# Performance work log

Measured on AMD Instinct MI355X. Metric: run time of the kernel, lower is better.

The kernel has to match this reference:

```python
import jax, jax.numpy as jnp
import numpy as np

N = 10000        # total nodes in batch
E = 320000       # total edges (before self-loops)
D_IN = 128       # node_dim
H_DIM = 64       # hidden_dim
HEADS = 4
B = 64           # number of graphs
NUM_EDGES = 1024 # actor output dim


def _lin(k, i, o):
    return jax.random.normal(k, (i, o), jnp.float32) / np.sqrt(i)


def setup_inputs() -> dict:
    key = jax.random.key(0)
    ks = jax.random.split(key, 32)
    x = jax.random.normal(ks[0], (N, D_IN), jnp.float32)
    edge_index = jax.random.randint(ks[1], (2, E), 0, N, dtype=jnp.int64)
    batch = jnp.sort(jax.random.randint(ks[2], (N,), 0, B, dtype=jnp.int64))
    inp = dict(x=x, edge_index=edge_index, batch=batch)
    # GAT layer 1: in=D_IN, heads=4, out=H_DIM, concat
    inp['W1'] = _lin(ks[3], D_IN, HEADS * H_DIM)
    inp['as1'] = jax.random.normal(ks[4], (HEADS, H_DIM), jnp.float32) * 0.1
    inp['ad1'] = jax.random.normal(ks[5], (HEADS, H_DIM), jnp.float32) * 0.1
    inp['b1'] = jnp.zeros((HEADS * H_DIM,), jnp.float32)
    # GAT layer 2: in=4*H_DIM, heads=4, out=H_DIM, concat
    inp['W2'] = _lin(ks[6], HEADS * H_DIM, HEADS * H_DIM)
    inp['as2'] = jax.random.normal(ks[7], (HEADS, H_DIM), jnp.float32) * 0.1
    inp['ad2'] = jax.random.normal(ks[8], (HEADS, H_DIM), jnp.float32) * 0.1
    inp['b2'] = jnp.zeros((HEADS * H_DIM,), jnp.float32)
    # GAT layer 3: in=4*H_DIM, heads=1, out=H_DIM, mean (concat=False)
    inp['W3'] = _lin(ks[9], HEADS * H_DIM, H_DIM)
    inp['as3'] = jax.random.normal(ks[10], (1, H_DIM), jnp.float32) * 0.1
    inp['ad3'] = jax.random.normal(ks[11], (1, H_DIM), jnp.float32) * 0.1
    inp['b3'] = jnp.zeros((H_DIM,), jnp.float32)
    # actor MLP
    inp['Wa1'] = _lin(ks[12], H_DIM, H_DIM); inp['ba1'] = jnp.zeros((H_DIM,), jnp.float32)
    inp['Wa2'] = _lin(ks[13], H_DIM, NUM_EDGES); inp['ba2'] = jnp.zeros((NUM_EDGES,), jnp.float32)
    # critic MLP
    inp['Wc1'] = _lin(ks[14], H_DIM, H_DIM); inp['bc1'] = jnp.zeros((H_DIM,), jnp.float32)
    inp['Wc2'] = _lin(ks[15], H_DIM, 1); inp['bc2'] = jnp.zeros((1,), jnp.float32)
    return inp


def gat_layer(x, src, dst, W, a_src, a_dst, bias, heads, out_dim, concat):
    # PyG GATConv: linear -> edge attention -> per-dst softmax -> scatter-add
    n = x.shape[0]
    h = (x @ W).reshape(n, heads, out_dim)            # [N,H,D]
    s = (h * a_src).sum(-1)                           # [N,H] attention src term
    d = (h * a_dst).sum(-1)                           # [N,H]
    e = jax.nn.leaky_relu(s[src] + d[dst], 0.2)       # [Eall,H]
    m = jax.ops.segment_max(e, dst, num_segments=n)   # stable softmax per dst node
    w = jnp.exp(e - m[dst])
    alpha = w / jax.ops.segment_sum(w, dst, num_segments=n)[dst]
    agg = jax.ops.segment_sum(h[src] * alpha[..., None], dst, num_segments=n)  # [N,H,D]
    o = agg.reshape(n, heads * out_dim) if concat else agg.mean(axis=1)
    return o + bias


def forward(x, edge_index, batch, W1, as1, ad1, b1, W2, as2, ad2, b2,
            W3, as3, ad3, b3, Wa1, ba1, Wa2, ba2, Wc1, bc1, Wc2, bc2):
    n = x.shape[0]
    loop = jnp.arange(n, dtype=edge_index.dtype)
    src = jnp.concatenate([edge_index[0], loop])      # add_self_loops=True (PyG default)
    dst = jnp.concatenate([edge_index[1], loop])
    h = jax.nn.relu(gat_layer(x, src, dst, W1, as1, ad1, b1, HEADS, H_DIM, True))
    h = jax.nn.relu(gat_layer(h, src, dst, W2, as2, ad2, b2, HEADS, H_DIM, True))
    h = jax.nn.relu(gat_layer(h, src, dst, W3, as3, ad3, b3, 1, H_DIM, False))
    # global_mean_pool
    counts = jax.ops.segment_sum(jnp.ones((n,), h.dtype), batch, num_segments=B)
    pooled = jax.ops.segment_sum(h, batch, num_segments=B) / jnp.maximum(counts, 1.0)[:, None]
    # heads (dropout is identity at inference)
    action = jnp.tanh(jax.nn.relu(pooled @ Wa1 + ba1) @ Wa2 + ba2)
    value = jax.nn.relu(pooled @ Wc1 + bc1) @ Wc2 + bc2
    return action, value


def reference(x, edge_index, batch, W1, as1, ad1, b1, W2, as2, ad2, b2,
              W3, as3, ad3, b3, Wa1, ba1, Wa2, ba2, Wc1, bc1, Wc2, bc2):
    return forward(x, edge_index, batch, W1, as1, ad1, b1, W2, as2, ad2, b2,
                   W3, as3, ad3, b3, Wa1, ba1, Wa2, ba2, Wc1, bc1, Wc2, bc2)
```

## Files before the change

### kernel.cpp

```cpp
#include <hip/hip_runtime.h>
#include <hip/hip_bf16.h>

#define NN 10000
#define EE 320000
#define EALL (EE + NN)
#define BG 64
#define AOUT 1024
#define CAP 128

#define WTOT 191361
#define SCB ((EALL + 255) / 256)

typedef __hip_bfloat16 bf16;
typedef __attribute__((ext_vector_type(8))) short bf16x8;
typedef __attribute__((ext_vector_type(4))) float f32x4;

__device__ __forceinline__ unsigned short f2bf(float f) {
    bf16 h = __float2bfloat16(f);
    return *reinterpret_cast<unsigned short*>(&h);
}
__device__ __forceinline__ float bf2f(unsigned short u) {
    bf16 h;
    *reinterpret_cast<unsigned short*>(&h) = u;
    return __bfloat162float(h);
}
__device__ __forceinline__ int iread(const void* p, int fi, long long idx) {
    return fi ? ((const int*)p)[idx] : (int)((const long long*)p)[idx];
}

struct WPtrs { const void* p[20]; };
#define CVT_TOT (WTOT + 32768 + 65536 + 16384 + NN)
__global__ __launch_bounds__(256) void k_cvt_all(WPtrs wp, const void* __restrict__ xsrc,
                          float* __restrict__ wf,
                          unsigned short* __restrict__ w1t, unsigned short* __restrict__ w2t,
                          unsigned short* __restrict__ w3t, int* __restrict__ cnt, int ffh) {
    __shared__ int sff;
    int ff = ffh;
    if (ffh < 0) {
        const int t = threadIdx.x;
        bool nanp = false;
        const uint4* xs4 = (const uint4*)xsrc;
        uint4 a = xs4[t * 8 + 0], b = xs4[t * 8 + 4];
        const unsigned int wds[8] = {a.x, a.y, a.z, a.w, b.x, b.y, b.z, b.w};
#pragma unroll
        for (int k = 0; k < 8; k++) {
            unsigned int w2 = wds[k];
            if ((w2 & 0x7F80u) == 0x7F80u || ((w2 >> 16) & 0x7F80u) == 0x7F80u) nanp = true;
        }
        unsigned long long bn = __ballot(nanp);
        if (t == 0) sff = 0;
        __syncthreads();
        if ((t & 63) == 0 && bn) atomicOr(&sff, 1);
        __syncthreads();
        ff = sff;
    }

    const int sz[20] = {32768,256,256,256,65536,256,256,256,16384,64,64,64,4096,64,65536,1024,4096,64,64,1};
    int i = blockIdx.x * 256 + threadIdx.x;
    if (i < WTOT) {
        int seg = 0, off = 0;
        while (i - off >= sz[seg]) { off += sz[seg]; seg++; }
        const void* src = wp.p[seg];
        int k = i - off;
        wf[i] = ff ? ((const float*)src)[k] : __bfloat162float(((const bf16*)src)[k]);
        return;
    }
    i -= WTOT;
    if (i < 32768) {
        int k = i >> 8, c = i & 255;
        float v = ff ? ((const float*)wp.p[0])[i] : __bfloat162float(((const bf16*)wp.p[0])[i]);
        w1t[c * 128 + k] = f2bf(v);
        return;
    }
    i -= 32768;
    if (i < 65536) {
        int k = i >> 8, c = i & 255;
        float v = ff ? ((const float*)wp.p[4])[i] : __bfloat162float(((const bf16*)wp.p[4])[i]);
        w2t[c * 256 + k] = f2bf(v);
        return;
    }
    i -= 65536;
    if (i < 16384) {
        int k = i >> 6, c = i & 63;
        float v = ff ? ((const float*)wp.p[8])[i] : __bfloat162float(((const bf16*)wp.p[8])[i]);
        w3t[c * 256 + k] = f2bf(v);
        return;
    }
    i -= 16384;
    if (i < NN) cnt[i] = 0;
}

__global__ __launch_bounds__(256) void k_fuse1(const void* __restrict__ eisrc,
                                               const void* __restrict__ xsrc,
                                               int ffh, int fih,
                                               int* __restrict__ cnt, int* __restrict__ ssrc,
                                               const unsigned short* __restrict__ WT16,
                                               const float* __restrict__ asf,
                                               const float* __restrict__ adf,
                                               unsigned short* __restrict__ C16,
                                               float* __restrict__ sb, float* __restrict__ db) {
    constexpr int LDW = 40;
    __shared__ alignas(16) char smem[10240];
    __shared__ int sff, sfi;
    const int t = threadIdx.x;
    int ff = ffh, fi = fih;
    if (ffh < 0 || fih < 0) {
        bool nanp = false, odd = false;
        const uint4* xs4 = (const uint4*)xsrc;
        uint4 a = xs4[t * 8 + 0], b = xs4[t * 8 + 4];
        const unsigned int wds[8] = {a.x, a.y, a.z, a.w, b.x, b.y, b.z, b.w};
#pragma unroll
        for (int k = 0; k < 8; k++) {
            unsigned int w2 = wds[k];
            if ((w2 & 0x7F80u) == 0x7F80u || ((w2 >> 16) & 0x7F80u) == 0x7F80u) nanp = true;
        }
        odd = ((const unsigned int*)eisrc)[2 * t + 1] != 0u;
        unsigned long long bn = __ballot(nanp);
        unsigned long long bo = __ballot(odd);
        if (t == 0) { sff = 0; sfi = 0; }
        __syncthreads();
        if ((t & 63) == 0) {
            if (bn) atomicOr(&sff, 1);
            if (bo) atomicOr(&sfi, 1);
        }
        __syncthreads();
        ff = (ffh >= 0) ? ffh : sff;
        fi = (fih >= 0) ? fih : sfi;
    }

    if (blockIdx.x < SCB) {
        int e = blockIdx.x * 256 + t;
        if (e < EALL) {
            int dst = (e < EE) ? iread(eisrc, fi, (long long)EE + e) : (e - EE);
            int src = (e < EE) ? iread(eisrc, fi, e) : dst;
            int pos = atomicAdd(&cnt[dst], 1);
            if (pos < CAP) ssrc[(size_t)dst * CAP + pos] = src;
        }
        return;
    }
    unsigned short* As = (unsigned short*)smem;
    unsigned short* Bs = As + 64 * LDW;
    constexpr int K = 128, M = 256, H = M / 64;
    const int u = blockIdx.x - SCB;
    const int bx = u % 157;
    const int hh = u / 157;
    const int row0 = bx * 64, col0 = hh * 64;
    const int wv = t >> 6, lane = t & 63;
    const int m = lane & 15, q = lane >> 4;
    const int srow = t >> 2, skoff = (t & 3) * 8;

    f32x4 acc[4] = {};
    for (int k0 = 0; k0 < K; k0 += 32) {
        {
            int grow = row0 + srow;
            uint4 av = make_uint4(0u, 0u, 0u, 0u);
            if (grow < NN) {
                if (ff) {
                    const float* xp = (const float*)xsrc + (size_t)grow * K + k0 + skoff;
                    float4 fa = *(const float4*)xp;
                    float4 fb = *(const float4*)(xp + 4);
                    union { unsigned short u16[8]; uint4 v; } pk;
                    pk.u16[0] = f2bf(fa.x); pk.u16[1] = f2bf(fa.y);
                    pk.u16[2] = f2bf(fa.z); pk.u16[3] = f2bf(fa.w);
                    pk.u16[4] = f2bf(fb.x); pk.u16[5] = f2bf(fb.y);
                    pk.u16[6] = f2bf(fb.z); pk.u16[7] = f2bf(fb.w);
                    av = pk.v;
                } else {
                    av = *(const uint4*)((const unsigned short*)xsrc + (size_t)grow * K + k0 + skoff);
                }
            }
            *(uint4*)&As[srow * LDW + skoff] = av;
            uint4 bv = *(const uint4*)&WT16[(size_t)(col0 + srow) * K + k0 + skoff];
            *(uint4*)&Bs[srow * LDW + skoff] = bv;
        }
        __syncthreads();
        bf16x8 af = *(const bf16x8*)&As[(16 * wv + m) * LDW + q * 8];
#pragma unroll
        for (int ct = 0; ct < 4; ct++) {
            bf16x8 bfv = *(const bf16x8*)&Bs[(16 * ct + m) * LDW + q * 8];
            acc[ct] = __builtin_amdgcn_mfma_f32_16x16x32_bf16(af, bfv, acc[ct], 0, 0, 0);
        }
        __syncthreads();
    }
    float asv[4], adv[4];
#pragma unroll
    for (int ct = 0; ct < 4; ct++) {
        asv[ct] = asf[hh * 64 + 16 * ct + m];
        adv[ct] = adf[hh * 64 + 16 * ct + m];
    }
#pragma unroll
    for (int reg = 0; reg < 4; reg++) {
        int row = row0 + 16 * wv + q * 4 + reg;
        float ps = 0.f, pd = 0.f;
        if (row < NN) {
#pragma unroll
            for (int ct = 0; ct < 4; ct++) {
                float v = acc[ct][reg];
                C16[(size_t)row * M + col0 + 16 * ct + m] = f2bf(v);
                ps += v * asv[ct];
                pd += v * adv[ct];
            }
        }
#pragma unroll
        for (int off = 1; off < 16; off <<= 1) {
            ps += __shfl_xor(ps, off);
            pd += __shfl_xor(pd, off);
        }
        if (m == 0 && row < NN) { sb[row * H + hh] = ps; db[row * H + hh] = pd; }
    }
}

template<int K, int M>
__global__ __launch_bounds__(256) void k_gemm(const unsigned short* __restrict__ A16,
                                              const unsigned short* __restrict__ WT16,
                                              const float* __restrict__ asf,
                                              const float* __restrict__ adf,
                                              unsigned short* __restrict__ C16,
                                              float* __restrict__ sb, float* __restrict__ db) {
    constexpr int BK = 32;
    constexpr int H = M / 64;
    constexpr int LDW = 40;
    __shared__ unsigned short As[64 * LDW];
    __shared__ unsigned short Bs[64 * LDW];
    const int row0 = blockIdx.x * 64;
    const int col0 = blockIdx.y * 64;
    const int hh = blockIdx.y;
    const int t = threadIdx.x;
    const int wv = t >> 6;
    const int lane = t & 63;
    const int m = lane & 15;
    const int q = lane >> 4;
    const int srow = t >> 2;
    const int skoff = (t & 3) * 8;

    f32x4 acc[4] = {};

    for (int k0 = 0; k0 < K; k0 += BK) {
        {
            int grow = row0 + srow;
            uint4 av = make_uint4(0u, 0u, 0u, 0u);
            if (grow < NN) av = *(const uint4*)&A16[(size_t)grow * K + k0 + skoff];
            *(uint4*)&As[srow * LDW + skoff] = av;
            uint4 bv = *(const uint4*)&WT16[(size_t)(col0 + srow) * K + k0 + skoff];
            *(uint4*)&Bs[srow * LDW + skoff] = bv;
        }
        __syncthreads();
        bf16x8 af = *(const bf16x8*)&As[(16 * wv + m) * LDW + q * 8];
#pragma unroll
        for (int ct = 0; ct < 4; ct++) {
            bf16x8 bfv = *(const bf16x8*)&Bs[(16 * ct + m) * LDW + q * 8];
            acc[ct] = __builtin_amdgcn_mfma_f32_16x16x32_bf16(af, bfv, acc[ct], 0, 0, 0);
        }
        __syncthreads();
    }

    float asv[4], adv[4];
#pragma unroll
    for (int ct = 0; ct < 4; ct++) {
        asv[ct] = asf[hh * 64 + 16 * ct + m];
        adv[ct] = adf[hh * 64 + 16 * ct + m];
    }
#pragma unroll
    for (int reg = 0; reg < 4; reg++) {
        int row = row0 + 16 * wv + q * 4 + reg;
        float ps = 0.f, pd = 0.f;
        if (row < NN) {
#pragma unroll
            for (int ct = 0; ct < 4; ct++) {
                float v = acc[ct][reg];
                C16[(size_t)row * M + col0 + 16 * ct + m] = f2bf(v);
                ps += v * asv[ct];
                pd += v * adv[ct];
            }
        }
#pragma unroll
        for (int off = 1; off < 16; off <<= 1) {
            ps += __shfl_xor(ps, off);
            pd += __shfl_xor(pd, off);
        }
        if (m == 0 && row < NN) { sb[row * H + hh] = ps; db[row * H + hh] = pd; }
    }
}

template<int H>
__global__ void k_agg(const unsigned short* __restrict__ hbuf16, const float* __restrict__ sb,
                      const float* __restrict__ db, const int* __restrict__ cnt,
                      const int* __restrict__ ssrc, const float* __restrict__ bias,
                      unsigned short* __restrict__ out16) {
    constexpr int M = H * 64;
    constexpr int NW = M / 64;
    constexpr int CG = M / 8;
    constexpr int LCG = (H == 4) ? 5 : 3;
    const int n = blockIdx.x;
    const int tid = threadIdx.x;
    const int start = n * CAP;
    const int end = start + min(cnt[n], CAP);
    const int wv = tid >> 6;
    const int lane = tid & 63;
    const int cg = tid & (CG - 1);
    const int eg = tid >> LCG;
    const int chh = (H == 4) ? (cg >> 3) : 0;
    __shared__ float accbuf[8 * M];
    __shared__ float sww[NW][H];
    const float dn = db[n * H + chh];

    float wsum = 0.f;
    float acc[8] = {};
#pragma unroll 4
    for (int p = start + eg; p < end; p += 8) {
        int s = ssrc[p];
        float e = sb[s * H + chh] + dn;
        e = e > 0.f ? e : 0.2f * e;
        float w2 = __expf(e);
        wsum += w2;
        const bf16x8 v = *(const bf16x8*)&hbuf16[(size_t)s * M + cg * 8];
#pragma unroll
        for (int i = 0; i < 8; i++)
            acc[i] += w2 * bf2f((unsigned short)v[i]);
    }

    {
        float* ab = &accbuf[eg * M + cg * 8];
#pragma unroll
        for (int i = 0; i < 8; i++) ab[i] = acc[i];
    }
    if constexpr (NW > 1) {
        wsum += __shfl_xor(wsum, 32);
        if (lane < 32 && (cg & 7) == 0) sww[wv][chh] = wsum;
    } else {
        wsum += __shfl_xor(wsum, 8);
        wsum += __shfl_xor(wsum, 16);
        wsum += __shfl_xor(wsum, 32);
    }
    __syncthreads();

    float wsh;
    if constexpr (NW > 1) {
        const int h2 = tid >> 6;
        wsh = sww[0][h2] + sww[1][h2] + sww[2][h2] + sww[3][h2];
    } else {
        wsh = wsum;
    }

    float o = 0.f;
#pragma unroll
    for (int e8 = 0; e8 < 8; e8++) o += accbuf[e8 * M + tid];
    o = o / wsh + bias[tid];
    out16[(size_t)n * M + tid] = f2bf(fmaxf(o, 0.f));
}

__global__ __launch_bounds__(256) void k_final(const unsigned short* __restrict__ feat16,
                                               const void* __restrict__ bsrc, int fih,
                                               const void* __restrict__ eisrc,
                                               const float* __restrict__ Wa1, const float* __restrict__ ba1,
                                               const float* __restrict__ Wc1, const float* __restrict__ bc1,
                                               const float* __restrict__ Wa2, const float* __restrict__ ba2,
                                               const float* __restrict__ Wc2, const float* __restrict__ bc2,
                                               float* __restrict__ out) {
    __shared__ float red[256];
    __shared__ float p[64];
    __shared__ float a[64], cc[64];
    __shared__ int sfi;
    const int g = blockIdx.x, t = threadIdx.x;
    int fi = fih;
    if (fih < 0) {
        bool odd = ((const unsigned int*)eisrc)[2 * t + 1] != 0u;
        unsigned long long bo = __ballot(odd);
        if (t == 0) sfi = 0;
        __syncthreads();
        if ((t & 63) == 0 && bo) atomicOr(&sfi, 1);
        __syncthreads();
        fi = sfi;
    }
    int s, e;
    {
        int lo = 0, hi = NN;
        while (lo < hi) { int mid = (lo + hi) >> 1; if (iread(bsrc, fi, mid) < g) lo = mid + 1; else hi = mid; }
        s = lo;
        lo = 0; hi = NN;
        while (lo < hi) { int mid = (lo + hi) >> 1; if (iread(bsrc, fi, mid) < g + 1) lo = mid + 1; else hi = mid; }
        e = lo;
    }
    const int d = t & 63, c = t >> 6;
    float acc = 0.f;
    for (int n = s + c; n < e; n += 4) acc += bf2f(feat16[(size_t)n * 64 + d]);
    red[t] = acc; __syncthreads();
    if (c == 0) p[d] = (red[d] + red[64 + d] + red[128 + d] + red[192 + d])
                       / fmaxf((float)(e - s), 1.f);
    __syncthreads();
    if (t < 128) {
        int j = t & 63;
        const float* W  = (t < 64) ? Wa1 : Wc1;
        const float* bb = (t < 64) ? ba1 : bc1;
        float h = 0.f;
#pragma unroll 8
        for (int k = 0; k < 64; k++) h += p[k] * W[k * 64 + j];
        h = fmaxf(h + bb[j], 0.f);
        if (t < 64) a[j] = h; else cc[j] = h;
    }
    __syncthreads();
    float o[4] = {0.f, 0.f, 0.f, 0.f};
    for (int k = 0; k < 64; k++) {
        float ak = a[k];
#pragma unroll
        for (int q = 0; q < 4; q++) o[q] += ak * Wa2[k * AOUT + t + 256 * q];
    }
#pragma unroll
    for (int q = 0; q < 4; q++)
        out[g * AOUT + t + 256 * q] = tanhf(o[q] + ba2[t + 256 * q]);
    if (t == 0) {
        float v = 0.f;
        for (int k = 0; k < 64; k++) v += cc[k] * Wc2[k];
        out[BG * AOUT + g] = v + bc2[0];
    }
}

extern "C" void kernel_launch(void* const* d_in, const int* in_sizes, int n_in,
                              void* d_out, int out_size, void* d_ws, size_t ws_size,
                              hipStream_t stream) {
    float* out = (float*)d_out;

    char* w = (char*)d_ws;
    auto alloc = [&](size_t bytes) { void* p = (void*)w; w += (bytes + 255) & ~size_t(255); return p; };
    float* wf      = (float*)alloc((size_t)WTOT * 4);
    unsigned short* w1t    = (unsigned short*)alloc((size_t)32768 * 2);
    unsigned short* w2t    = (unsigned short*)alloc((size_t)65536 * 2);
    unsigned short* w3t    = (unsigned short*)alloc((size_t)16384 * 2);
    unsigned short* actA16 = (unsigned short*)alloc((size_t)NN * 256 * 2);
    unsigned short* actB16 = (unsigned short*)alloc((size_t)NN * 256 * 2);
    float* sb      = (float*)alloc((size_t)NN * 4 * 4);
    float* db      = (float*)alloc((size_t)NN * 4 * 4);
    int*   cnt     = (int*)alloc((size_t)NN * 4);
    int*   ssrc    = (int*)alloc((size_t)NN * CAP * 4);

    int ffh = -1, fih = -1;
    if (in_sizes && n_in >= 2) {
        long long xs = in_sizes[0];
        if (xs == (long long)NN * 128 * 4) ffh = 1;
        else if (xs == (long long)NN * 128 * 2) ffh = 0;
        long long es = in_sizes[1];
        if (es == (long long)2 * EE * 8) fih = 0;
        else if (es == (long long)2 * EE * 4) fih = 1;
    }

    WPtrs wp;
    for (int s = 0; s < 20; s++) wp.p[s] = d_in[3 + s];
    k_cvt_all<<<(CVT_TOT + 255) / 256, 256, 0, stream>>>(
        wp, d_in[0], wf, w1t, w2t, w3t, cnt, ffh);

    const int wsz[20] = {32768,256,256,256,65536,256,256,256,16384,64,64,64,4096,64,65536,1024,4096,64,64,1};
    int woff[20]; int acc = 0;
    for (int s = 0; s < 20; s++) { woff[s] = acc; acc += wsz[s]; }
    const float *as1f = wf + woff[1], *ad1f = wf + woff[2], *b1f = wf + woff[3];
    const float *as2f = wf + woff[5], *ad2f = wf + woff[6], *b2f = wf + woff[7];
    const float *as3f = wf + woff[9], *ad3f = wf + woff[10], *b3f = wf + woff[11];
    const float *Wa1f = wf + woff[12], *ba1f = wf + woff[13], *Wa2f = wf + woff[14], *ba2f = wf + woff[15];
    const float *Wc1f = wf + woff[16], *bc1f = wf + woff[17], *Wc2f = wf + woff[18], *bc2f = wf + woff[19];

    k_fuse1<<<SCB + 628, 256, 0, stream>>>(d_in[1], d_in[0], ffh, fih, cnt, ssrc,
                                           w1t, as1f, ad1f, actA16, sb, db);

    k_agg<4><<<NN, 256, 0, stream>>>(actA16, sb, db, cnt, ssrc, b1f, actB16);

    k_gemm<256, 256><<<dim3(157, 4), 256, 0, stream>>>(actB16, w2t, as2f, ad2f, actA16, sb, db);
    k_agg<4><<<NN, 256, 0, stream>>>(actA16, sb, db, cnt, ssrc, b2f, actB16);

    k_gemm<256, 64><<<dim3(157, 1), 256, 0, stream>>>(actB16, w3t, as3f, ad3f, actA16, sb, db);
    k_agg<1><<<NN, 64, 0, stream>>>(actA16, sb, db, cnt, ssrc, b3f, actB16);

    k_final<<<BG, 256, 0, stream>>>(actB16, d_in[2], fih, d_in[1],
                                    Wa1f, ba1f, Wc1f, bc1f, Wa2f, ba2f, Wc2f, bc2f, out);
}
```

Measured before the change: 224.5 us.

## Widen aggregation blocks, pack layer-3 nodes per block, skip large weight conversion

The 4-head aggregation now runs 512 threads per node with 16 edge groups, which is meant to expose more memory parallelism per node. The single-head aggregation packs four nodes per 256-thread block, one wave each, and drops the block-level sync, which is meant to raise occupancy and shrink the grid. The conversion kernel now converts only the small attention and bias vectors. The head MLP weights are read directly in their native dtype inside the final kernel, which now also detects the dtype itself, so the bulk fp32 copy of about 190K weights goes away. In exchange, half the threads in each 4-head block sit idle during the final reduction, and the final kernel carries extra dtype-branching code.

Result: slower. 238.2 us (+6.1%).

```diff
diff --git a/kernel.cpp b/kernel.cpp
--- a/kernel.cpp
+++ b/kernel.cpp
@@ -8,7 +8,6 @@
 #define AOUT 1024
 #define CAP 128
 
-#define WTOT 191361
 #define SCB ((EALL + 255) / 256)
 
 typedef __hip_bfloat16 bf16;
@@ -27,11 +26,14 @@
 __device__ __forceinline__ int iread(const void* p, int fi, long long idx) {
     return fi ? ((const int*)p)[idx] : (int)((const long long*)p)[idx];
 }
+__device__ __forceinline__ float fread1(const void* p, int ff, int idx) {
+    return ff ? ((const float*)p)[idx] : bf2f(((const unsigned short*)p)[idx]);
+}
 
 struct WPtrs { const void* p[20]; };
-#define CVT_TOT (WTOT + 32768 + 65536 + 16384 + NN)
+#define CVT_TOT (1728 + 32768 + 65536 + 16384 + NN)
 __global__ __launch_bounds__(256) void k_cvt_all(WPtrs wp, const void* __restrict__ xsrc,
-                          float* __restrict__ wf,
+                          float* __restrict__ wfv,
                           unsigned short* __restrict__ w1t, unsigned short* __restrict__ w2t,
                           unsigned short* __restrict__ w3t, int* __restrict__ cnt, int ffh) {
     __shared__ int sff;
@@ -55,34 +57,35 @@
         ff = sff;
     }
 
-    const int sz[20] = {32768,256,256,256,65536,256,256,256,16384,64,64,64,4096,64,65536,1024,4096,64,64,1};
     int i = blockIdx.x * 256 + threadIdx.x;
-    if (i < WTOT) {
+    if (i < 1728) {
+        const int vsz[9]  = {256,256,256,256,256,256,64,64,64};
+        const int vwp[9]  = {1,2,3,5,6,7,9,10,11};
+        const int voff[9] = {0,256,512,768,1024,1280,1536,1600,1664};
         int seg = 0, off = 0;
-        while (i - off >= sz[seg]) { off += sz[seg]; seg++; }
-        const void* src = wp.p[seg];
+        while (i - off >= vsz[seg]) { off += vsz[seg]; seg++; }
         int k = i - off;
-        wf[i] = ff ? ((const float*)src)[k] : __bfloat162float(((const bf16*)src)[k]);
+        wfv[voff[seg] + k] = fread1(wp.p[vwp[seg]], ff, k);
         return;
     }
-    i -= WTOT;
+    i -= 1728;
     if (i < 32768) {
         int k = i >> 8, c = i & 255;
-        float v = ff ? ((const float*)wp.p[0])[i] : __bfloat162float(((const bf16*)wp.p[0])[i]);
+        float v = fread1(wp.p[0], ff, i);
         w1t[c * 128 + k] = f2bf(v);
         return;
     }
     i -= 32768;
     if (i < 65536) {
         int k = i >> 8, c = i & 255;
-        float v = ff ? ((const float*)wp.p[4])[i] : __bfloat162float(((const bf16*)wp.p[4])[i]);
+        float v = fread1(wp.p[4], ff, i);
         w2t[c * 256 + k] = f2bf(v);
         return;
     }
     i -= 65536;
     if (i < 16384) {
         int k = i >> 6, c = i & 63;
-        float v = ff ? ((const float*)wp.p[8])[i] : __bfloat162float(((const bf16*)wp.p[8])[i]);
+        float v = fread1(wp.p[8], ff, i);
         w3t[c * 256 + k] = f2bf(v);
         return;
     }
@@ -282,95 +285,144 @@
     }
 }
 
-template<int H>
-__global__ void k_agg(const unsigned short* __restrict__ hbuf16, const float* __restrict__ sb,
-                      const float* __restrict__ db, const int* __restrict__ cnt,
-                      const int* __restrict__ ssrc, const float* __restrict__ bias,
-                      unsigned short* __restrict__ out16) {
-    constexpr int M = H * 64;
-    constexpr int NW = M / 64;
-    constexpr int CG = M / 8;
-    constexpr int LCG = (H == 4) ? 5 : 3;
+__global__ __launch_bounds__(512) void k_agg4(const unsigned short* __restrict__ hbuf16,
+                                              const float* __restrict__ sb,
+                                              const float* __restrict__ db,
+                                              const int* __restrict__ cnt,
+                                              const int* __restrict__ ssrc,
+                                              const float* __restrict__ bias,
+                                              unsigned short* __restrict__ out16) {
     const int n = blockIdx.x;
     const int tid = threadIdx.x;
     const int start = n * CAP;
     const int end = start + min(cnt[n], CAP);
-    const int wv = tid >> 6;
-    const int lane = tid & 63;
-    const int cg = tid & (CG - 1);
-    const int eg = tid >> LCG;
-    const int chh = (H == 4) ? (cg >> 3) : 0;
-    __shared__ float accbuf[8 * M];
-    __shared__ float sww[NW][H];
-    const float dn = db[n * H + chh];
-
+    const int wv = tid >> 6, lane = tid & 63;
+    const int cg = tid & 31;
+    const int eg = tid >> 5;
+    const int chh = cg >> 3;
+    __shared__ float accbuf[16 * 256];
+    __shared__ float sww[8][4];
+    const float dn = db[n * 4 + chh];
+
+    float wsum = 0.f;
+    float acc[8] = {};
+#pragma unroll 2
+    for (int p = start + eg; p < end; p += 16) {
+        int s = ssrc[p];
+        float e = sb[s * 4 + chh] + dn;
+        e = e > 0.f ? e : 0.2f * e;
+        float w2 = __expf(e);
+        wsum += w2;
+        const bf16x8 v = *(const bf16x8*)&hbuf16[(size_t)s * 256 + cg * 8];
+#pragma unroll
+        for (int i = 0; i < 8; i++)
+            acc[i] += w2 * bf2f((unsigned short)v[i]);
+    }
+    {
+        float* ab = &accbuf[eg * 256 + cg * 8];
+#pragma unroll
+        for (int i = 0; i < 8; i++) ab[i] = acc[i];
+    }
+    wsum += __shfl_xor(wsum, 32);
+    if (lane < 32 && (cg & 7) == 0) sww[wv][chh] = wsum;
+    __syncthreads();
+
+    if (tid < 256) {
+        const int h2 = tid >> 6;
+        float wsh = 0.f;
+#pragma unroll
+        for (int wq = 0; wq < 8; wq++) wsh += sww[wq][h2];
+        float o = 0.f;
+#pragma unroll
+        for (int e8 = 0; e8 < 16; e8++) o += accbuf[e8 * 256 + tid];
+        o = o / wsh + bias[tid];
+        out16[(size_t)n * 256 + tid] = f2bf(fmaxf(o, 0.f));
+    }
+}
+
+__global__ __launch_bounds__(256) void k_agg1w(const unsigned short* __restrict__ hbuf16,
+                                               const float* __restrict__ sb,
+                                               const float* __restrict__ db,
+                                               const int* __restrict__ cnt,
+                                               const int* __restrict__ ssrc,
+                                               const float* __restrict__ bias,
+                                               unsigned short* __restrict__ out16) {
+    __shared__ float accb[4 * 512];
+    const int tid = threadIdx.x;
+    const int wv = tid >> 6, lane = tid & 63;
+    const int eg = lane >> 3, cg = lane & 7;
+    const int n = blockIdx.x * 4 + wv;
+    if (n >= NN) return;
+    const int start = n * CAP;
+    const int end = start + min(cnt[n], CAP);
+    const float dn = db[n];
     float wsum = 0.f;
     float acc[8] = {};
 #pragma unroll 4
     for (int p = start + eg; p < end; p += 8) {
         int s = ssrc[p];
-        float e = sb[s * H + chh] + dn;
+        float e = sb[s] + dn;
         e = e > 0.f ? e : 0.2f * e;
         float w2 = __expf(e);
         wsum += w2;
-        const bf16x8 v = *(const bf16x8*)&hbuf16[(size_t)s * M + cg * 8];
+        const bf16x8 v = *(const bf16x8*)&hbuf16[(size_t)s * 64 + cg * 8];
 #pragma unroll
         for (int i = 0; i < 8; i++)
             acc[i] += w2 * bf2f((unsigned short)v[i]);
     }
-
     {
-        float* ab = &accbuf[eg * M + cg * 8];
+        float* ab = &accb[wv * 512 + eg * 64 + cg * 8];
 #pragma unroll
         for (int i = 0; i < 8; i++) ab[i] = acc[i];
     }
-    if constexpr (NW > 1) {
-        wsum += __shfl_xor(wsum, 32);
-        if (lane < 32 && (cg & 7) == 0) sww[wv][chh] = wsum;
-    } else {
-        wsum += __shfl_xor(wsum, 8);
-        wsum += __shfl_xor(wsum, 16);
-        wsum += __shfl_xor(wsum, 32);
-    }
-    __syncthreads();
-
-    float wsh;
-    if constexpr (NW > 1) {
-        const int h2 = tid >> 6;
-        wsh = sww[0][h2] + sww[1][h2] + sww[2][h2] + sww[3][h2];
-    } else {
-        wsh = wsum;
-    }
-
+    wsum += __shfl_xor(wsum, 8);
+    wsum += __shfl_xor(wsum, 16);
+    wsum += __shfl_xor(wsum, 32);
     float o = 0.f;
 #pragma unroll
-    for (int e8 = 0; e8 < 8; e8++) o += accbuf[e8 * M + tid];
-    o = o / wsh + bias[tid];
-    out16[(size_t)n * M + tid] = f2bf(fmaxf(o, 0.f));
+    for (int e8 = 0; e8 < 8; e8++) o += accb[wv * 512 + e8 * 64 + lane];
+    o = o / wsum + bias[lane];
+    out16[(size_t)n * 64 + lane] = f2bf(fmaxf(o, 0.f));
 }
 
 __global__ __launch_bounds__(256) void k_final(const unsigned short* __restrict__ feat16,
-                                               const void* __restrict__ bsrc, int fih,
+                                               const void* __restrict__ bsrc,
                                                const void* __restrict__ eisrc,
-                                               const float* __restrict__ Wa1, const float* __restrict__ ba1,
-                                               const float* __restrict__ Wc1, const float* __restrict__ bc1,
-                                               const float* __restrict__ Wa2, const float* __restrict__ ba2,
-                                               const float* __restrict__ Wc2, const float* __restrict__ bc2,
+                                               const void* __restrict__ xsrc,
+                                               int ffh, int fih,
+                                               const void* __restrict__ Wa1, const void* __restrict__ ba1,
+                                               const void* __restrict__ Wa2, const void* __restrict__ ba2,
+                                               const void* __restrict__ Wc1, const void* __restrict__ bc1,
+                                               const void* __restrict__ Wc2, const void* __restrict__ bc2,
                                                float* __restrict__ out) {
     __shared__ float red[256];
     __shared__ float p[64];
     __shared__ float a[64], cc[64];
-    __shared__ int sfi;
+    __shared__ int sff, sfi;
     const int g = blockIdx.x, t = threadIdx.x;
-    int fi = fih;
-    if (fih < 0) {
-        bool odd = ((const unsigned int*)eisrc)[2 * t + 1] != 0u;
+    int ff = ffh, fi = fih;
+    if (ffh < 0 || fih < 0) {
+        bool nanp = false, odd = false;
+        const uint4* xs4 = (const uint4*)xsrc;
+        uint4 av = xs4[t * 8 + 0], bv = xs4[t * 8 + 4];
+        const unsigned int wds[8] = {av.x, av.y, av.z, av.w, bv.x, bv.y, bv.z, bv.w};
+#pragma unroll
+        for (int k = 0; k < 8; k++) {
+            unsigned int w2 = wds[k];
+            if ((w2 & 0x7F80u) == 0x7F80u || ((w2 >> 16) & 0x7F80u) == 0x7F80u) nanp = true;
+        }
+        odd = ((const unsigned int*)eisrc)[2 * t + 1] != 0u;
+        unsigned long long bn = __ballot(nanp);
         unsigned long long bo = __ballot(odd);
-        if (t == 0) sfi = 0;
-        __syncthreads();
-        if ((t & 63) == 0 && bo) atomicOr(&sfi, 1);
-        __syncthreads();
-        fi = sfi;
+        if (t == 0) { sff = 0; sfi = 0; }
+        __syncthreads();
+        if ((t & 63) == 0) {
+            if (bn) atomicOr(&sff, 1);
+            if (bo) atomicOr(&sfi, 1);
+        }
+        __syncthreads();
+        ff = (ffh >= 0) ? ffh : sff;
+        fi = (fih >= 0) ? fih : sfi;
     }
     int s, e;
     {
@@ -390,28 +442,45 @@
     __syncthreads();
     if (t < 128) {
         int j = t & 63;
-        const float* W  = (t < 64) ? Wa1 : Wc1;
-        const float* bb = (t < 64) ? ba1 : bc1;
+        const void* W  = (t < 64) ? Wa1 : Wc1;
+        const void* bb = (t < 64) ? ba1 : bc1;
         float h = 0.f;
+        if (ff) {
+            const float* Wf = (const float*)W;
 #pragma unroll 8
-        for (int k = 0; k < 64; k++) h += p[k] * W[k * 64 + j];
-        h = fmaxf(h + bb[j], 0.f);
+            for (int k = 0; k < 64; k++) h += p[k] * Wf[k * 64 + j];
+        } else {
+            const unsigned short* Wh = (const unsigned short*)W;
+#pragma unroll 8
+            for (int k = 0; k < 64; k++) h += p[k] * bf2f(Wh[k * 64 + j]);
+        }
+        h = fmaxf(h + fread1(bb, ff, j), 0.f);
         if (t < 64) a[j] = h; else cc[j] = h;
     }
     __syncthreads();
     float o[4] = {0.f, 0.f, 0.f, 0.f};
-    for (int k = 0; k < 64; k++) {
-        float ak = a[k];
-#pragma unroll
-        for (int q = 0; q < 4; q++) o[q] += ak * Wa2[k * AOUT + t + 256 * q];
+    if (ff) {
+        const float* Wf = (const float*)Wa2;
+        for (int k = 0; k < 64; k++) {
+            float ak = a[k];
+#pragma unroll
+            for (int q = 0; q < 4; q++) o[q] += ak * Wf[k * AOUT + t + 256 * q];
+        }
+    } else {
+        const unsigned short* Wh = (const unsigned short*)Wa2;
+        for (int k = 0; k < 64; k++) {
+            float ak = a[k];
+#pragma unroll
+            for (int q = 0; q < 4; q++) o[q] += ak * bf2f(Wh[k * AOUT + t + 256 * q]);
+        }
     }
 #pragma unroll
     for (int q = 0; q < 4; q++)
-        out[g * AOUT + t + 256 * q] = tanhf(o[q] + ba2[t + 256 * q]);
+        out[g * AOUT + t + 256 * q] = tanhf(o[q] + fread1(ba2, ff, t + 256 * q));
     if (t == 0) {
         float v = 0.f;
-        for (int k = 0; k < 64; k++) v += cc[k] * Wc2[k];
-        out[BG * AOUT + g] = v + bc2[0];
+        for (int k = 0; k < 64; k++) v += cc[k] * fread1(Wc2, ff, k);
+        out[BG * AOUT + g] = v + fread1(bc2, ff, 0);
     }
 }
 
@@ -422,7 +491,7 @@
 
     char* w = (char*)d_ws;
     auto alloc = [&](size_t bytes) { void* p = (void*)w; w += (bytes + 255) & ~size_t(255); return p; };
-    float* wf      = (float*)alloc((size_t)WTOT * 4);
+    float* wfv     = (float*)alloc((size_t)1728 * 4);
     unsigned short* w1t    = (unsigned short*)alloc((size_t)32768 * 2);
     unsigned short* w2t    = (unsigned short*)alloc((size_t)65536 * 2);
     unsigned short* w3t    = (unsigned short*)alloc((size_t)16384 * 2);
@@ -446,28 +515,24 @@
     WPtrs wp;
     for (int s = 0; s < 20; s++) wp.p[s] = d_in[3 + s];
     k_cvt_all<<<(CVT_TOT + 255) / 256, 256, 0, stream>>>(
-        wp, d_in[0], wf, w1t, w2t, w3t, cnt, ffh);
-
-    const int wsz[20] = {32768,256,256,256,65536,256,256,256,16384,64,64,64,4096,64,65536,1024,4096,64,64,1};
-    int woff[20]; int acc = 0;
-    for (int s = 0; s < 20; s++) { woff[s] = acc; acc += wsz[s]; }
-    const float *as1f = wf + woff[1], *ad1f = wf + woff[2], *b1f = wf + woff[3];
-    const float *as2f = wf + woff[5], *ad2f = wf + woff[6], *b2f = wf + woff[7];
-    const float *as3f = wf + woff[9], *ad3f = wf + woff[10], *b3f = wf + woff[11];
-    const float *Wa1f = wf + woff[12], *ba1f = wf + woff[13], *Wa2f = wf + woff[14], *ba2f = wf + woff[15];
-    const float *Wc1f = wf + woff[16], *bc1f = wf + woff[17], *Wc2f = wf + woff[18], *bc2f = wf + woff[19];
+        wp, d_in[0], wfv, w1t, w2t, w3t, cnt, ffh);
+
+    const float *as1f = wfv + 0,   *ad1f = wfv + 256,  *b1f = wfv + 512;
+    const float *as2f = wfv + 768, *ad2f = wfv + 1024, *b2f = wfv + 1280;
+    const float *as3f = wfv + 1536,*ad3f = wfv + 1600, *b3f = wfv + 1664;
 
     k_fuse1<<<SCB + 628, 256, 0, stream>>>(d_in[1], d_in[0], ffh, fih, cnt, ssrc,
                                            w1t, as1f, ad1f, actA16, sb, db);
 
-    k_agg<4><<<NN, 256, 0, stream>>>(actA16, sb, db, cnt, ssrc, b1f, actB16);
+    k_agg4<<<NN, 512, 0, stream>>>(actA16, sb, db, cnt, ssrc, b1f, actB16);
 
     k_gemm<256, 256><<<dim3(157, 4), 256, 0, stream>>>(actB16, w2t, as2f, ad2f, actA16, sb, db);
-    k_agg<4><<<NN, 256, 0, stream>>>(actA16, sb, db, cnt, ssrc, b2f, actB16);
+    k_agg4<<<NN, 512, 0, stream>>>(actA16, sb, db, cnt, ssrc, b2f, actB16);
 
     k_gemm<256, 64><<<dim3(157, 1), 256, 0, stream>>>(actB16, w3t, as3f, ad3f, actA16, sb, db);
-    k_agg<1><<<NN, 64, 0, stream>>>(actA16, sb, db, cnt, ssrc, b3f, actB16);
-
-    k_final<<<BG, 256, 0, stream>>>(actB16, d_in[2], fih, d_in[1],
-                                    Wa1f, ba1f, Wc1f, bc1f, Wa2f, ba2f, Wc2f, bc2f, out);
-}
+    k_agg1w<<<(NN + 3) / 4, 256, 0, stream>>>(actA16, sb, db, cnt, ssrc, b3f, actB16);
+
+    k_final<<<BG, 256, 0, stream>>>(actB16, d_in[2], d_in[1], d_in[0], ffh, fih,
+                                    d_in[15], d_in[16], d_in[17], d_in[18],
+                                    d_in[19], d_in[20], d_in[21], d_in[22], out);
+}
```
